# Kernel tuning notes

Hardware: AMD Instinct MI355X
Metric: run time of the kernel (lower is better)

Reference implementation:

```python
import jax, jax.numpy as jnp
import numpy as np

B, S, R, H = 32, 512, 196, 1024


def setup_inputs() -> dict:
    key = jax.random.key(0)
    ks = jax.random.split(key, 12)
    sc = 1.0 / np.sqrt(H)
    return {
        "dns_feature": jax.random.normal(ks[0], (B, S, H), jnp.float32),
        "img_features": jax.random.normal(ks[1], (B, R, H), jnp.float32),
        # attention 1 params (dns_linear_1 has bias, img_linear_1 does not)
        "W_d1": jax.random.normal(ks[2], (H, H), jnp.float32) * sc,
        "b_d1": jax.random.normal(ks[3], (H,), jnp.float32) * sc,
        "W_i1": jax.random.normal(ks[4], (H, H), jnp.float32) * sc,
        "w_att1": jax.random.normal(ks[5], (2 * H,), jnp.float32) * sc,
        "b_att1": jax.random.normal(ks[6], (), jnp.float32) * sc,
        # attention 2 params (img_linear_2 has bias, dns_linear_2 does not)
        "W_d2": jax.random.normal(ks[7], (H, H), jnp.float32) * sc,
        "W_i2": jax.random.normal(ks[8], (H, H), jnp.float32) * sc,
        "b_i2": jax.random.normal(ks[9], (H,), jnp.float32) * sc,
        "w_att2": jax.random.normal(ks[10], (2 * H,), jnp.float32) * sc,
        "b_att2": jax.random.normal(ks[11], (), jnp.float32) * sc,
    }


def reference(dns_feature, img_features, W_d1, b_d1, W_i1, w_att1, b_att1,
              W_d2, W_i2, b_i2, w_att2, b_att2):
    h = dns_feature.shape[-1]
    # --- attention 1: dns attends over image regions ---
    # original: tanh(concat(Lin(dns_rep), Lin(img_rep))) -> att_linear_1.
    # tanh is elementwise and the concat linear is separable, so
    # score[b,s,r] = wA . tanh(W_d1 dns[b,s] + b_d1) + wB . tanh(W_i1 img[b,r]) + b_att1
    dns_p = jnp.tanh(jnp.einsum('bsh,oh->bso', dns_feature, W_d1) + b_d1)   # (B,S,H)
    img_p = jnp.tanh(jnp.einsum('brh,oh->bro', img_features, W_i1))          # (B,R,H)
    wA, wB = w_att1[:h], w_att1[h:]
    scores1 = (jnp.einsum('bsh,h->bs', dns_p, wA)[:, :, None]
               + jnp.einsum('brh,h->br', img_p, wB)[:, None, :] + b_att1)    # (B,S,R)
    visual_att = jax.nn.softmax(scores1, axis=-1)
    att_img_features = jnp.einsum('bsr,brh->bsh', visual_att, img_features)  # (B,S,H)
    # --- attention 2: attended image (per token i) attends over dns tokens j ---
    # concat order is [img_proj, dns_proj] here.
    img_p2 = jnp.tanh(jnp.einsum('bih,oh->bio', att_img_features, W_i2) + b_i2)  # (B,S,H)
    dns_p2 = jnp.tanh(jnp.einsum('bjh,oh->bjo', dns_feature, W_d2))              # (B,S,H)
    wI, wD = w_att2[:h], w_att2[h:]
    scores2 = (jnp.einsum('bih,h->bi', img_p2, wI)[:, :, None]
               + jnp.einsum('bjh,h->bj', dns_p2, wD)[:, None, :] + b_att2)       # (B,S,S)
    textual_att = jax.nn.softmax(scores2, axis=-1)
    att_dns_features = jnp.einsum('bij,bjh->bih', textual_att, dns_feature)      # (B,S,H)
    return att_dns_features, att_img_features
```

## Files before the change

### kernel.cpp

```cpp
#include <hip/hip_runtime.h>
#include <hip/hip_bf16.h>
#include <stdint.h>

typedef __bf16 bh;
typedef __bf16 bf16x8 __attribute__((ext_vector_type(8)));
typedef float f32x4 __attribute__((ext_vector_type(4)));

#define B_  32
#define S_  512
#define R_  196
#define H_  1024
#define BH  (B_ * H_)


__device__ __forceinline__ float fast_tanh(float x) {
  x = fminf(10.f, fmaxf(-10.f, x));
  float e = __expf(2.f * x);
  return (e - 1.f) / (e + 1.f);
}

__device__ __forceinline__ bf16x8 cvt8(const float4 a, const float4 b) {
  bf16x8 r;
  r[0] = (bh)a.x; r[1] = (bh)a.y; r[2] = (bh)a.z; r[3] = (bh)a.w;
  r[4] = (bh)b.x; r[5] = (bh)b.y; r[6] = (bh)b.z; r[7] = (bh)b.w;
  return r;
}

__device__ __forceinline__ void gload_lds16(const bh* g, bh* l) {
  __builtin_amdgcn_global_load_lds(
      (__attribute__((address_space(1))) void*)g,
      (__attribute__((address_space(3))) void*)l,
      16, 0, 0);
}

#define G_DNS 2097152
#define G_IMG 802816
#define G_W   131072
#define G_TOT (G_DNS + G_IMG + 2 * G_W)

__global__ __launch_bounds__(256)
void convert_kernel(const float* __restrict__ dns, const float* __restrict__ img,
                    const float* __restrict__ Wd2, const float* __restrict__ Wi1,
                    bh* __restrict__ dnsB, bh* __restrict__ imgB,
                    bh* __restrict__ wd2B, bh* __restrict__ wi1B) {
  for (int g = blockIdx.x * 256 + threadIdx.x; g < G_TOT; g += gridDim.x * 256) {
    const float* src; bh* dst; int off;
    if (g < G_DNS)                    { src = dns; dst = dnsB; off = g; }
    else if (g < G_DNS + G_IMG)       { src = img; dst = imgB; off = g - G_DNS; }
    else if (g < G_DNS + G_IMG + G_W) { src = Wd2; dst = wd2B; off = g - G_DNS - G_IMG; }
    else                              { src = Wi1; dst = wi1B; off = g - G_DNS - G_IMG - G_W; }
    float4 a = ((const float4*)src)[(size_t)off * 2];
    float4 b = ((const float4*)src)[(size_t)off * 2 + 1];
    ((bf16x8*)dst)[off] = cvt8(a, b);
  }
}


__global__ __launch_bounds__(256, 4)
void score_gemm_kernel(const bh* __restrict__ dnsB, const bh* __restrict__ imgB,
                       const bh* __restrict__ Wd2B, const bh* __restrict__ Wi1B,
                       const float* __restrict__ watt1, const float* __restrict__ watt2,
                       float* __restrict__ sPartD, float* __restrict__ sPartB) {
  __shared__ __align__(16) bh As[2][128 * 32];
  __shared__ __align__(16) bh Bs[2][128 * 32];
  __shared__ float sred[128];

  const int tid = threadIdx.x;
  const int wave = tid >> 6, lane = tid & 63;

  const int d = blockIdx.x;
  const int k = (d & 7) * 177 + (d >> 3);
  const int my = k >> 3, ny = k & 7;

  const bh* X; const bh* W; const float* w; float* sp; int m0;
  if (my < 128) { X = dnsB; W = Wd2B; w = watt2 + H_; sp = sPartD; m0 = my * 128; }
  else          { X = imgB; W = Wi1B; w = watt1 + H_; sp = sPartB; m0 = (my - 128) * 128; }
  const int n0 = ny * 128;

  const int srow  = wave * 32 + (lane >> 2);
  const int ssege = (((lane & 3) ^ ((lane >> 3) & 3)) * 8);
  const bh* Ag = X + ((size_t)(m0 + srow) * H_ + ssege);
  const bh* Bg = W + ((size_t)(n0 + srow) * H_ + ssege);
  const int lw = wave * 32 * 32;

  const int wm = wave >> 1, wn = wave & 1;
  const int col = lane & 15, quad = lane >> 4;
  const int qx8 = ((quad ^ ((col >> 1) & 3)) * 8);

  f32x4 acc[4][4] = {};

  gload_lds16(Ag,            &As[0][lw]);
  gload_lds16(Ag + 16 * H_,  &As[0][lw + 16 * 32]);
  gload_lds16(Bg,            &Bs[0][lw]);
  gload_lds16(Bg + 16 * H_,  &Bs[0][lw + 16 * 32]);
  __syncthreads();

  for (int kt = 0; kt < 32; ++kt) {
    const int cur = kt & 1;
    if (kt + 1 < 32) {
      const int ko = (kt + 1) * 32;
      gload_lds16(Ag + ko,            &As[cur ^ 1][lw]);
      gload_lds16(Ag + ko + 16 * H_,  &As[cur ^ 1][lw + 16 * 32]);
      gload_lds16(Bg + ko,            &Bs[cur ^ 1][lw]);
      gload_lds16(Bg + ko + 16 * H_,  &Bs[cur ^ 1][lw + 16 * 32]);
    }

    bf16x8 af[4], bfr[4];
#pragma unroll
    for (int mi = 0; mi < 4; ++mi)
      af[mi] = *(const bf16x8*)(&As[cur][(wm * 64 + mi * 16 + col) * 32 + qx8]);
#pragma unroll
    for (int ni = 0; ni < 4; ++ni)
      bfr[ni] = *(const bf16x8*)(&Bs[cur][(wn * 64 + ni * 16 + col) * 32 + qx8]);

#pragma unroll
    for (int mi = 0; mi < 4; ++mi)
#pragma unroll
      for (int ni = 0; ni < 4; ++ni)
        acc[mi][ni] = __builtin_amdgcn_mfma_f32_16x16x32_bf16(af[mi], bfr[ni], acc[mi][ni], 0, 0, 0);

    __syncthreads();
  }

  float wv[4];
#pragma unroll
  for (int ni = 0; ni < 4; ++ni) wv[ni] = w[n0 + wn * 64 + ni * 16 + col];

  float ppv[4][4];
#pragma unroll
  for (int mi = 0; mi < 4; ++mi) {
#pragma unroll
    for (int reg = 0; reg < 4; ++reg) {
      float pp = 0.f;
#pragma unroll
      for (int ni = 0; ni < 4; ++ni) pp += fast_tanh(acc[mi][ni][reg]) * wv[ni];
      pp += __shfl_xor(pp, 1);
      pp += __shfl_xor(pp, 2);
      pp += __shfl_xor(pp, 4);
      pp += __shfl_xor(pp, 8);
      ppv[mi][reg] = pp;
    }
  }

  if (wn == 0 && col == 0) {
#pragma unroll
    for (int mi = 0; mi < 4; ++mi)
#pragma unroll
      for (int reg = 0; reg < 4; ++reg)
        sred[wm * 64 + mi * 16 + quad * 4 + reg] = ppv[mi][reg];
  }
  __syncthreads();
  if (wn == 1 && col == 0) {
#pragma unroll
    for (int mi = 0; mi < 4; ++mi)
#pragma unroll
      for (int reg = 0; reg < 4; ++reg) {
        int ml = wm * 64 + mi * 16 + quad * 4 + reg;
        sp[(size_t)(m0 + ml) * 8 + ny] = sred[ml] + ppv[mi][reg];
      }
  }
}

__global__ __launch_bounds__(256)
void wsum_bcast_kernel(const float* __restrict__ dns, const float* __restrict__ img,
                       const float* __restrict__ sPartD, const float* __restrict__ sPartB,
                       float* __restrict__ out) {
  __shared__ float red[4];
  __shared__ float esd[512];
  __shared__ float esi[196];
  __shared__ float4 aru[4][16];
  __shared__ float4 arv[4][16];
  __shared__ float4 su[16], sv[16];

  const int b = blockIdx.x, hc = blockIdx.y;
  const int tid = threadIdx.x, wave = tid >> 6, lane = tid & 63;
  float inv_d, inv_i;

  {
    const float4* p4 = (const float4*)(sPartD + (size_t)b * S_ * 8);
    float4 a0 = p4[tid * 2],         a1 = p4[tid * 2 + 1];
    float4 c0 = p4[(tid + 256) * 2], c1 = p4[(tid + 256) * 2 + 1];
    float x0 = a0.x + a0.y + a0.z + a0.w + a1.x + a1.y + a1.z + a1.w;
    float x1 = c0.x + c0.y + c0.z + c0.w + c1.x + c1.y + c1.z + c1.w;
    float m = fmaxf(x0, x1);
#pragma unroll
    for (int msk = 32; msk; msk >>= 1) m = fmaxf(m, __shfl_xor(m, msk));
    if (!lane) red[wave] = m;
    __syncthreads();
    float bm = fmaxf(fmaxf(red[0], red[1]), fmaxf(red[2], red[3]));
    __syncthreads();
    float e0 = __expf(x0 - bm), e1 = __expf(x1 - bm);
    esd[tid] = e0; esd[tid + 256] = e1;
    float s = e0 + e1;
#pragma unroll
    for (int msk = 32; msk; msk >>= 1) s += __shfl_xor(s, msk);
    if (!lane) red[wave] = s;
    __syncthreads();
    inv_d = 1.f / (red[0] + red[1] + red[2] + red[3]);
    __syncthreads();
  }
  {
    float x = -3.0e38f;
    if (tid < R_) {
      const float4* p4 = (const float4*)(sPartB + (size_t)b * R_ * 8);
      float4 a0 = p4[tid * 2], a1 = p4[tid * 2 + 1];
      x = a0.x + a0.y + a0.z + a0.w + a1.x + a1.y + a1.z + a1.w;
    }
    float m = x;
#pragma unroll
    for (int msk = 32; msk; msk >>= 1) m = fmaxf(m, __shfl_xor(m, msk));
    if (!lane) red[wave] = m;
    __syncthreads();
    float bm = fmaxf(fmaxf(red[0], red[1]), fmaxf(red[2], red[3]));
    __syncthreads();
    float e = (tid < R_) ? __expf(x - bm) : 0.f;
    if (tid < R_) esi[tid] = e;
    float s = e;
#pragma unroll
    for (int msk = 32; msk; msk >>= 1) s += __shfl_xor(s, msk);
    if (!lane) red[wave] = s;
    __syncthreads();
    inv_i = 1.f / (red[0] + red[1] + red[2] + red[3]);
    __syncthreads();
  }

  const int h4 = tid & 15, jg = tid >> 4;
  const float* db = dns + (size_t)b * S_ * H_ + hc * 64 + h4 * 4;
  float4 ua = {0.f, 0.f, 0.f, 0.f};
#pragma unroll
  for (int it = 0; it < 32; ++it) {
    const int j = jg + it * 16;
    float4 xv = *(const float4*)(db + (size_t)j * H_);
    float qv = esd[j];
    ua.x += qv * xv.x; ua.y += qv * xv.y; ua.z += qv * xv.z; ua.w += qv * xv.w;
  }
  const float* ib = img + (size_t)b * R_ * H_ + hc * 64 + h4 * 4;
  float4 va = {0.f, 0.f, 0.f, 0.f};
#pragma unroll
  for (int it = 0; it < 13; ++it) {
    const int j = jg + it * 16;
    if (j < R_) {
      float4 xv = *(const float4*)(ib + (size_t)j * H_);
      float pv = esi[j];
      va.x += pv * xv.x; va.y += pv * xv.y; va.z += pv * xv.z; va.w += pv * xv.w;
    }
  }
#pragma unroll
  for (int msk = 16; msk <= 32; msk <<= 1) {
    ua.x += __shfl_xor(ua.x, msk); ua.y += __shfl_xor(ua.y, msk);
    ua.z += __shfl_xor(ua.z, msk); ua.w += __shfl_xor(ua.w, msk);
    va.x += __shfl_xor(va.x, msk); va.y += __shfl_xor(va.y, msk);
    va.z += __shfl_xor(va.z, msk); va.w += __shfl_xor(va.w, msk);
  }
  if (lane < 16) { aru[wave][lane] = ua; arv[wave][lane] = va; }
  __syncthreads();
  if (tid < 16) {
    float4 s0 = aru[0][tid], s1 = aru[1][tid], s2 = aru[2][tid], s3 = aru[3][tid];
    float4 r;
    r.x = (s0.x + s1.x + s2.x + s3.x) * inv_d;
    r.y = (s0.y + s1.y + s2.y + s3.y) * inv_d;
    r.z = (s0.z + s1.z + s2.z + s3.z) * inv_d;
    r.w = (s0.w + s1.w + s2.w + s3.w) * inv_d;
    su[tid] = r;
    s0 = arv[0][tid]; s1 = arv[1][tid]; s2 = arv[2][tid]; s3 = arv[3][tid];
    r.x = (s0.x + s1.x + s2.x + s3.x) * inv_i;
    r.y = (s0.y + s1.y + s2.y + s3.y) * inv_i;
    r.z = (s0.z + s1.z + s2.z + s3.z) * inv_i;
    r.w = (s0.w + s1.w + s2.w + s3.w) * inv_i;
    sv[tid] = r;
  }
  __syncthreads();

  const int PER4 = B_ * S_ * H_ / 4;
  const float4 u4 = su[h4], v4 = sv[h4];
  float4* o0 = (float4*)out + ((size_t)b * S_ + jg) * 256 + hc * 16 + h4;
  float4* o1 = o0 + PER4;
#pragma unroll
  for (int s = 0; s < 32; ++s) {
    o0[(size_t)s * 16 * 256] = u4;
    o1[(size_t)s * 16 * 256] = v4;
  }
}


extern "C" void kernel_launch(void* const* d_in, const int* in_sizes, int n_in,
                              void* d_out, int out_size, void* d_ws, size_t ws_size,
                              hipStream_t stream) {
  const float* dns   = (const float*)d_in[0];
  const float* img   = (const float*)d_in[1];
  const float* Wi1   = (const float*)d_in[4];
  const float* watt1 = (const float*)d_in[5];
  const float* Wd2   = (const float*)d_in[7];
  const float* watt2 = (const float*)d_in[10];
  float* out = (float*)d_out;

  float* ws = (float*)d_ws;
  float* sPartD = ws;
  float* sPartB = ws + 131072;
  bh* dnsB = (bh*)(ws + 181248);
  bh* imgB = (bh*)(ws + 8569856);
  bh* wd2B = (bh*)(ws + 11781120);
  bh* wi1B = (bh*)(ws + 12305408);

  convert_kernel<<<2048, 256, 0, stream>>>(dns, img, Wd2, Wi1, dnsB, imgB, wd2B, wi1B);
  score_gemm_kernel<<<1416, 256, 0, stream>>>(
      dnsB, imgB, wd2B, wi1B, watt1, watt2, sPartD, sPartB);
  wsum_bcast_kernel<<<dim3(B_, 16), 256, 0, stream>>>(dns, img, sPartD, sPartB, out);
}
```

Baseline: 323.5 us.

## Restructure score GEMM main loop with explicit vmcnt waits and MFMA priority

The score GEMM's K-loop is rewritten so two stages are prefetched up front. Each iteration reads its fragments into registers, waits on LDS, then barriers and immediately reissues the next global-to-LDS load into the same buffer before running the MFMAs. Partial vmcnt waits replace full __syncthreads drains, and s_setprio raises wave priority around the MFMA block. The intent is to overlap global loads with matrix compute and cut barrier stalls, at the cost of hand-managed waitcnt logic that could race if the counts are wrong.

After: 320.5 us (median of 2 runs). Within noise of the previous version (-0.9%).

```diff
diff --git a/kernel.cpp b/kernel.cpp
--- a/kernel.cpp
+++ b/kernel.cpp
@@ -56,6 +56,26 @@
 }
 
 
+__device__ __forceinline__ void frag_load(const bh* Asb, const bh* Bsb,
+                                          int abase, int bbase,
+                                          bf16x8 af[4], bf16x8 bfr[4]) {
+#pragma unroll
+  for (int mi = 0; mi < 4; ++mi) af[mi]  = *(const bf16x8*)(Asb + abase + mi * 16 * 32);
+#pragma unroll
+  for (int ni = 0; ni < 4; ++ni) bfr[ni] = *(const bf16x8*)(Bsb + bbase + ni * 16 * 32);
+}
+
+__device__ __forceinline__ void mfma16(const bf16x8 af[4], const bf16x8 bfr[4],
+                                       f32x4 acc[4][4]) {
+  __builtin_amdgcn_s_setprio(1);
+#pragma unroll
+  for (int mi = 0; mi < 4; ++mi)
+#pragma unroll
+    for (int ni = 0; ni < 4; ++ni)
+      acc[mi][ni] = __builtin_amdgcn_mfma_f32_16x16x32_bf16(af[mi], bfr[ni], acc[mi][ni], 0, 0, 0);
+  __builtin_amdgcn_s_setprio(0);
+}
+
 __global__ __launch_bounds__(256, 4)
 void score_gemm_kernel(const bh* __restrict__ dnsB, const bh* __restrict__ imgB,
                        const bh* __restrict__ Wd2B, const bh* __restrict__ Wi1B,
@@ -86,41 +106,48 @@
   const int wm = wave >> 1, wn = wave & 1;
   const int col = lane & 15, quad = lane >> 4;
   const int qx8 = ((quad ^ ((col >> 1) & 3)) * 8);
+  const int abase = (wm * 64 + col) * 32 + qx8;
+  const int bbase = (wn * 64 + col) * 32 + qx8;
 
   f32x4 acc[4][4] = {};
 
-  gload_lds16(Ag,            &As[0][lw]);
-  gload_lds16(Ag + 16 * H_,  &As[0][lw + 16 * 32]);
-  gload_lds16(Bg,            &Bs[0][lw]);
-  gload_lds16(Bg + 16 * H_,  &Bs[0][lw + 16 * 32]);
-  __syncthreads();
-
-  for (int kt = 0; kt < 32; ++kt) {
-    const int cur = kt & 1;
-    if (kt + 1 < 32) {
-      const int ko = (kt + 1) * 32;
-      gload_lds16(Ag + ko,            &As[cur ^ 1][lw]);
-      gload_lds16(Ag + ko + 16 * H_,  &As[cur ^ 1][lw + 16 * 32]);
-      gload_lds16(Bg + ko,            &Bs[cur ^ 1][lw]);
-      gload_lds16(Bg + ko + 16 * H_,  &Bs[cur ^ 1][lw + 16 * 32]);
-    }
-
+#define STAGE(buf, kt) {                                        \
+    const int ko_ = (kt) * 32;                                  \
+    gload_lds16(Ag + ko_,           &As[buf][lw]);              \
+    gload_lds16(Ag + ko_ + 16 * H_, &As[buf][lw + 16 * 32]);    \
+    gload_lds16(Bg + ko_,           &Bs[buf][lw]);              \
+    gload_lds16(Bg + ko_ + 16 * H_, &Bs[buf][lw + 16 * 32]); }
+
+  STAGE(0, 0);
+  STAGE(1, 1);
+  asm volatile("s_waitcnt vmcnt(4)" ::: "memory");
+  __builtin_amdgcn_s_barrier();
+
+  for (int t = 0; t < 30; ++t) {
+    const int cur = t & 1;
     bf16x8 af[4], bfr[4];
-#pragma unroll
-    for (int mi = 0; mi < 4; ++mi)
-      af[mi] = *(const bf16x8*)(&As[cur][(wm * 64 + mi * 16 + col) * 32 + qx8]);
-#pragma unroll
-    for (int ni = 0; ni < 4; ++ni)
-      bfr[ni] = *(const bf16x8*)(&Bs[cur][(wn * 64 + ni * 16 + col) * 32 + qx8]);
-
-#pragma unroll
-    for (int mi = 0; mi < 4; ++mi)
-#pragma unroll
-      for (int ni = 0; ni < 4; ++ni)
-        acc[mi][ni] = __builtin_amdgcn_mfma_f32_16x16x32_bf16(af[mi], bfr[ni], acc[mi][ni], 0, 0, 0);
-
-    __syncthreads();
-  }
+    frag_load(As[cur], Bs[cur], abase, bbase, af, bfr);
+    asm volatile("s_waitcnt lgkmcnt(0)" ::: "memory");
+    __builtin_amdgcn_sched_barrier(0);
+    __builtin_amdgcn_s_barrier();
+    STAGE(cur, t + 2);
+    mfma16(af, bfr, acc);
+    asm volatile("s_waitcnt vmcnt(4)" ::: "memory");
+    __builtin_amdgcn_s_barrier();
+  }
+  {
+    bf16x8 af[4], bfr[4];
+    frag_load(As[0], Bs[0], abase, bbase, af, bfr);
+    mfma16(af, bfr, acc);
+    asm volatile("s_waitcnt vmcnt(0)" ::: "memory");
+    __builtin_amdgcn_s_barrier();
+  }
+  {
+    bf16x8 af[4], bfr[4];
+    frag_load(As[1], Bs[1], abase, bbase, af, bfr);
+    mfma16(af, bfr, acc);
+  }
+#undef STAGE
 
   float wv[4];
 #pragma unroll
```
